# Kernel tuning notes

Measured on AMD Instinct MI355X. Metric: run time of the kernel, lower is better.

## Reference

```python
import jax, jax.numpy as jnp
import numpy as np

CTX = 768   # ctx_len in the original module
C = 768     # n_embd
B = 16
T = 768
K_EPS = 1e-8


def setup_inputs() -> dict:
    key = jax.random.key(0)
    ks = jax.random.split(key, 10)
    scale = 1.0 / np.sqrt(C)
    x = jax.random.normal(ks[0], (B, T, C), jnp.float32)
    time_decay = jax.random.normal(ks[1], (C, 1), jnp.float32) * 0.1
    time_first = jnp.full((C, 1), np.log(0.3), jnp.float32)
    time_mix_k = jax.random.uniform(ks[2], (1, 1, C), jnp.float32)
    time_mix_v = jax.random.uniform(ks[3], (1, 1, C), jnp.float32)
    time_mix_r = jax.random.uniform(ks[4], (1, 1, C), jnp.float32)
    Wk = jax.random.normal(ks[5], (C, C), jnp.float32) * scale
    Wv = jax.random.normal(ks[6], (C, C), jnp.float32) * scale
    Wr = jax.random.normal(ks[7], (C, C), jnp.float32) * scale
    Wo = jax.random.normal(ks[8], (C, C), jnp.float32) * scale
    return {"x": x, "time_decay": time_decay, "time_first": time_first,
            "time_mix_k": time_mix_k, "time_mix_v": time_mix_v, "time_mix_r": time_mix_r,
            "Wk": Wk, "Wv": Wv, "Wr": Wr, "Wo": Wo}


def reference(x, time_decay, time_first, time_mix_k, time_mix_v, time_mix_r, Wk, Wv, Wr, Wo):
    Bb, Tt, Cc = x.shape
    # time_shift: xx[t] = x[t-1], xx[0] = 0
    xx = jnp.pad(x, ((0, 0), (1, 0), (0, 0)))[:, :Tt]
    xk = x * time_mix_k + xx * (1.0 - time_mix_k)
    xv = x * time_mix_v + xx * (1.0 - time_mix_v)
    xr = x * time_mix_r + xx * (1.0 - time_mix_r)
    # projections (nn.Linear, no bias: y = x @ W.T); k, v laid out [B, C, T]
    k = jnp.einsum('btc,oc->bot', xk, Wk)
    v = jnp.einsum('btc,oc->bot', xv, Wv)
    r = jnp.einsum('btc,oc->bto', xr, Wr)
    k = jnp.exp(jnp.minimum(k, 60.0))
    kv = k * v
    # decay kernel: time_w = cat([exp(time_decay)*time_curve, time_first]); w = exp(time_w)[:, -T:]
    curve = (jnp.arange(CTX - 1) - (CTX - 2)).astype(x.dtype)  # [-(CTX-2) .. 0]
    tw = jnp.concatenate([jnp.exp(time_decay) * curve[None, :], time_first], axis=-1)  # [C, CTX]
    w = jnp.exp(tw)[:, -Tt:]            # [C, T]
    kern = w[:, None, :]                # [C, 1, T] depthwise kernel

    def causal_conv(z):  # z: [B, C, T] -> [B, C, T], left-padded cross-correlation
        return jax.lax.conv_general_dilated(
            z, kern, window_strides=(1,), padding=[(Tt - 1, 0)],
            feature_group_count=Cc, dimension_numbers=('NCH', 'OIH', 'NCH'))

    wkv = causal_conv(kv)
    wk = causal_conv(k) + K_EPS
    rwkv = jax.nn.sigmoid(r) * jnp.transpose(wkv / wk, (0, 2, 1))  # [B, T, C]
    return jnp.einsum('btc,oc->bto', rwkv, Wo)
```

## Files before the change

### kernel.cpp

```cpp
#include <hip/hip_runtime.h>
#include <math.h>

#define Mq 12288
#define Nq 768
#define Kq 768
#define Tq 768
#define Bq 16
#define Cq 768
#define BK 64
#define BM 128

typedef __bf16 bf16x8 __attribute__((ext_vector_type(8)));
typedef __bf16 bf16x4 __attribute__((ext_vector_type(4)));
typedef __bf16 bf16x2 __attribute__((ext_vector_type(2)));
typedef float  floatx4 __attribute__((ext_vector_type(4)));

#define GLD_LDS16(g, l) __builtin_amdgcn_global_load_lds(                      \
    (const __attribute__((address_space(1))) unsigned int*)(g),                \
    (__attribute__((address_space(3))) unsigned int*)(l), 16, 0, 0)

__global__ __launch_bounds__(256)
void prep_kernel(const float* __restrict__ x,
                 const float* __restrict__ mk, const float* __restrict__ mv,
                 const float* __restrict__ mr,
                 const float* __restrict__ Wk, const float* __restrict__ Wv,
                 const float* __restrict__ Wr, const float* __restrict__ Wo,
                 __bf16* __restrict__ xk, __bf16* __restrict__ xv,
                 __bf16* __restrict__ xr, __bf16* __restrict__ wp)
{
    const int bid = blockIdx.x;
    if (bid < 9216) {
        const int i  = bid * 256 + threadIdx.x;
        const int c4 = i % (Cq / 4);
        const int m  = i / (Cq / 4);
        const int t  = m % Tq;
        const int c0 = c4 * 4;

        const float4 xc = *(const float4*)(x + (size_t)m * Cq + c0);
        float4 xp = make_float4(0.f, 0.f, 0.f, 0.f);
        if (t > 0) xp = *(const float4*)(x + (size_t)(m - 1) * Cq + c0);

        const float4 k4 = *(const float4*)(mk + c0);
        const float4 v4 = *(const float4*)(mv + c0);
        const float4 r4 = *(const float4*)(mr + c0);

        bf16x4 ok = { (__bf16)fmaf(k4.x, xc.x - xp.x, xp.x),
                      (__bf16)fmaf(k4.y, xc.y - xp.y, xp.y),
                      (__bf16)fmaf(k4.z, xc.z - xp.z, xp.z),
                      (__bf16)fmaf(k4.w, xc.w - xp.w, xp.w) };
        bf16x4 ov = { (__bf16)fmaf(v4.x, xc.x - xp.x, xp.x),
                      (__bf16)fmaf(v4.y, xc.y - xp.y, xp.y),
                      (__bf16)fmaf(v4.z, xc.z - xp.z, xp.z),
                      (__bf16)fmaf(v4.w, xc.w - xp.w, xp.w) };
        bf16x4 orr = { (__bf16)fmaf(r4.x, xc.x - xp.x, xp.x),
                       (__bf16)fmaf(r4.y, xc.y - xp.y, xp.y),
                       (__bf16)fmaf(r4.z, xc.z - xp.z, xp.z),
                       (__bf16)fmaf(r4.w, xc.w - xp.w, xp.w) };
        const size_t o = (size_t)m * Cq + c0;
        *(bf16x4*)(xk + o) = ok;
        *(bf16x4*)(xv + o) = ov;
        *(bf16x4*)(xr + o) = orr;
    } else {
        const int i   = (bid - 9216) * 256 + threadIdx.x;
        const int a   = i / 147456;
        const int off = (i - a * 147456) * 4;
        const float* s = (a == 0) ? Wk : (a == 1) ? Wv : (a == 2) ? Wr : Wo;
        const float4 v = *(const float4*)(s + off);
        bf16x4 r = { (__bf16)v.x, (__bf16)v.y, (__bf16)v.z, (__bf16)v.w };
        *(bf16x4*)(wp + (size_t)a * 589824 + off) = r;
    }
}

template<bool KVR>
__global__ __launch_bounds__(256, 3)
void mfma_gemm(const __bf16* __restrict__ A0, const __bf16* __restrict__ A1,
               const __bf16* __restrict__ A2,
               const __bf16* __restrict__ W,
               __bf16* __restrict__ OUTb, float* __restrict__ OUTf)
{
    __shared__ __bf16 As[BM * BK];
    __shared__ __bf16 Bs[128 * BK];

    const int STRIPS = KVR ? 18 : 6;

    const int i_    = blockIdx.x;
    const int xcd   = i_ & 7;
    const int j_    = i_ >> 3;
    const int strip = j_ % STRIPS;
    const int mt    = xcd * 12 + j_ / STRIPS;

    const int tid   = threadIdx.x;
    const int wave  = tid >> 6;
    const int lane  = tid & 63;
    const int m0    = mt * BM;
    const int matid = KVR ? strip / 6 : 0;
    const int n0    = KVR ? (strip % 6) * 128 : strip * 128;
    const int wn0   = strip * 128;

    const __bf16* A = KVR ? (matid == 0 ? A0 : matid == 1 ? A1 : A2) : A0;

    const int r8 = lane >> 3;
    const int sc = (lane & 7) ^ r8;
    const __bf16* gA[4];  __bf16* lA[4];
    const __bf16* gB[4];  __bf16* lB[4];
#pragma unroll
    for (int i = 0; i < 4; ++i) {
        const int row = (wave * 4 + i) * 8 + r8;
        gA[i] = A + (size_t)(m0 + row) * Kq + sc * 8;
        lA[i] = As + (wave * 4 + i) * 512;
        gB[i] = W + (size_t)(wn0 + row) * Kq + sc * 8;
        lB[i] = Bs + (wave * 4 + i) * 512;
    }

    const int wm   = wave & 1;
    const int wn   = wave >> 1;
    const int xRow = wm * 64 + (lane & 15);
    const int wRow = wn * 64 + (lane & 15);
    const int lk   = lane >> 4;

    floatx4 acc[4][4];
#pragma unroll
    for (int i = 0; i < 4; ++i)
#pragma unroll
        for (int j = 0; j < 4; ++j) acc[i][j] = (floatx4){0.f, 0.f, 0.f, 0.f};

    for (int kt = 0; kt < Kq / BK; ++kt) {
#pragma unroll
        for (int i = 0; i < 4; ++i) { GLD_LDS16(gA[i], lA[i]); gA[i] += BK; }
#pragma unroll
        for (int i = 0; i < 4; ++i) { GLD_LDS16(gB[i], lB[i]); gB[i] += BK; }
        __syncthreads();

#pragma unroll
        for (int kk = 0; kk < 2; ++kk) {
            bf16x8 wF[4], xF[4];
#pragma unroll
            for (int i = 0; i < 4; ++i) {
                const int r = wRow + i * 16;
                wF[i] = *(const bf16x8*)(Bs + r * BK +
                                         (((kk << 2) | lk) ^ (r & 7)) * 8);
            }
#pragma unroll
            for (int j = 0; j < 4; ++j) {
                const int r = xRow + j * 16;
                xF[j] = *(const bf16x8*)(As + r * BK +
                                         (((kk << 2) | lk) ^ (r & 7)) * 8);
            }
#pragma unroll
            for (int i = 0; i < 4; ++i)
#pragma unroll
                for (int j = 0; j < 4; ++j)
                    acc[i][j] = __builtin_amdgcn_mfma_f32_16x16x32_bf16(
                        wF[i], xF[j], acc[i][j], 0, 0, 0);
        }
        __syncthreads();
    }

#pragma unroll
    for (int j = 0; j < 4; ++j) {
        const int tok = m0 + wm * 64 + j * 16 + (lane & 15);
#pragma unroll
        for (int i = 0; i < 4; ++i) {
            const int ch = n0 + wn * 64 + i * 16 + (lane >> 4) * 4;
            if (KVR) {
                float v0 = acc[i][j][0], v1 = acc[i][j][1];
                float v2 = acc[i][j][2], v3 = acc[i][j][3];
                if (matid == 0) {
                    v0 = expf(fminf(v0, 60.f)); v1 = expf(fminf(v1, 60.f));
                    v2 = expf(fminf(v2, 60.f)); v3 = expf(fminf(v3, 60.f));
                } else if (matid == 2) {
                    v0 = 1.f / (1.f + expf(-v0)); v1 = 1.f / (1.f + expf(-v1));
                    v2 = 1.f / (1.f + expf(-v2)); v3 = 1.f / (1.f + expf(-v3));
                }
                bf16x4 o = { (__bf16)v0, (__bf16)v1, (__bf16)v2, (__bf16)v3 };
                *(bf16x4*)(OUTb + (size_t)matid * Mq * Nq +
                           (size_t)tok * Nq + ch) = o;
            } else {
                floatx4 o = acc[i][j];
                *(floatx4*)(OUTf + (size_t)tok * Nq + ch) = o;
            }
        }
    }
}

#define SEG 16
#define SLEN (Tq / SEG)

__global__ __launch_bounds__(1024)
void scan_kernel(const __bf16* __restrict__ kb, const __bf16* __restrict__ vb,
                 __bf16* rb,
                 const float* __restrict__ td, const float* __restrict__ tf)
{
    __shared__ float2 aS[SEG][64];
    __shared__ float2 bS[SEG][64];

    const int cx  = threadIdx.x;
    const int seg = threadIdx.y;
    const int c0  = blockIdx.x * 128 + cx * 2;
    const int b   = blockIdx.y;

    const float d0 = expf(td[c0]),     d1 = expf(td[c0 + 1]);
    const float w0 = expf(-d0),        w1 = expf(-d1);
    const float u0 = expf(tf[c0]),     u1 = expf(tf[c0 + 1]);

    const size_t base = ((size_t)b * Tq + seg * SLEN) * Cq + c0;

    float a0 = 0.f, a1 = 0.f, s0 = 0.f, s1 = 0.f;
#pragma unroll 4
    for (int t = 0; t < SLEN; ++t) {
        const size_t idx = base + (size_t)t * Cq;
        const bf16x2 k2 = *(const bf16x2*)(kb + idx);
        const bf16x2 v2 = *(const bf16x2*)(vb + idx);
        const float k0 = (float)k2[0], k1 = (float)k2[1];
        a0 = fmaf(w0, a0, k0 * (float)v2[0]);
        a1 = fmaf(w1, a1, k1 * (float)v2[1]);
        s0 = fmaf(w0, s0, k0);
        s1 = fmaf(w1, s1, k1);
    }
    aS[seg][cx] = make_float2(a0, a1);
    bS[seg][cx] = make_float2(s0, s1);
    __syncthreads();

    if (seg == 0) {
        const float W0 = expf(-d0 * (float)SLEN);
        const float W1 = expf(-d1 * (float)SLEN);
        float ia0 = 0.f, ia1 = 0.f, ib0 = 0.f, ib1 = 0.f;
#pragma unroll
        for (int s = 0; s < SEG; ++s) {
            const float2 ta = aS[s][cx];
            const float2 tb = bS[s][cx];
            aS[s][cx] = make_float2(ia0, ia1);
            bS[s][cx] = make_float2(ib0, ib1);
            ia0 = fmaf(W0, ia0, ta.x);  ia1 = fmaf(W1, ia1, ta.y);
            ib0 = fmaf(W0, ib0, tb.x);  ib1 = fmaf(W1, ib1, tb.y);
        }
    }
    __syncthreads();

    const float2 ain = aS[seg][cx];
    const float2 bin = bS[seg][cx];
    a0 = ain.x; a1 = ain.y; s0 = bin.x; s1 = bin.y;
#pragma unroll 2
    for (int t = 0; t < SLEN; ++t) {
        const size_t idx = base + (size_t)t * Cq;
        const bf16x2 k2 = *(const bf16x2*)(kb + idx);
        const bf16x2 v2 = *(const bf16x2*)(vb + idx);
        const bf16x2 r2 = *(const bf16x2*)(rb + idx);
        const float k0 = (float)k2[0], k1 = (float)k2[1];
        const float kv0 = k0 * (float)v2[0], kv1 = k1 * (float)v2[1];
        const float n0 = fmaf(u0, kv0, a0), n1 = fmaf(u1, kv1, a1);
        const float e0 = fmaf(u0, k0, s0) + 1e-8f;
        const float e1 = fmaf(u1, k1, s1) + 1e-8f;
        bf16x2 o = { (__bf16)((float)r2[0] * n0 / e0),
                     (__bf16)((float)r2[1] * n1 / e1) };
        *(bf16x2*)(rb + idx) = o;
        a0 = fmaf(w0, a0, kv0);  a1 = fmaf(w1, a1, kv1);
        s0 = fmaf(w0, s0, k0);   s1 = fmaf(w1, s1, k1);
    }
}

extern "C" void kernel_launch(void* const* d_in, const int* in_sizes, int n_in,
                              void* d_out, int out_size, void* d_ws, size_t ws_size,
                              hipStream_t stream)
{
    const float* x  = (const float*)d_in[0];
    const float* td = (const float*)d_in[1];
    const float* tf = (const float*)d_in[2];
    const float* mk = (const float*)d_in[3];
    const float* mv = (const float*)d_in[4];
    const float* mr = (const float*)d_in[5];
    const float* Wk = (const float*)d_in[6];
    const float* Wv = (const float*)d_in[7];
    const float* Wr = (const float*)d_in[8];
    const float* Wo = (const float*)d_in[9];

    const size_t MC = (size_t)Mq * Cq;

    __bf16* xk = (__bf16*)d_out;
    __bf16* xv = xk + MC;

    __bf16* xr   = (__bf16*)d_ws;
    __bf16* kbuf = xr + MC;
    __bf16* vbuf = kbuf + MC;
    __bf16* rbuf = vbuf + MC;
    __bf16* Wp   = rbuf + MC;
    __bf16* Wob  = Wp + 3 * 589824;

    prep_kernel<<<11520, 256, 0, stream>>>(x, mk, mv, mr, Wk, Wv, Wr, Wo,
                                           xk, xv, xr, Wp);

    mfma_gemm<true><<<18 * 96, 256, 0, stream>>>(
        xk, xv, xr, Wp, kbuf, nullptr);

    scan_kernel<<<dim3(Cq / 128, Bq), dim3(64, SEG), 0, stream>>>(
        kbuf, vbuf, rbuf, td, tf);

    mfma_gemm<false><<<6 * 96, 256, 0, stream>>>(
        rbuf, nullptr, nullptr, Wob, nullptr, (float*)d_out);
}
```

Measured before the change: 227.2 us.

## Triple-buffer GEMM LDS with 8-wave 128x256 tiles and split-phase prefetch

The bf16 MFMA GEMM goes from 256-thread 128x128 tiles with a single LDS buffer and full syncs to 512-thread 128x256 tiles. A three-stage ring of LDS buffers is filled by direct global-to-LDS loads issued two K-steps ahead, split across two half-steps with explicit vmcnt waits and barriers. s_setprio brackets the MFMA bursts. This hides global-load latency and halves the number of blocks, at the cost of more LDS per block, lower occupancy and tighter synchronisation that may be fragile.

New measurement: 243.4 us. 7.1% more time.

```diff
diff --git a/kernel.cpp b/kernel.cpp
--- a/kernel.cpp
+++ b/kernel.cpp
@@ -9,6 +9,9 @@
 #define Cq 768
 #define BK 64
 #define BM 128
+#define BN 256
+#define KT (Kq / BK)
+#define BUFE 24576
 
 typedef __bf16 bf16x8 __attribute__((ext_vector_type(8)));
 typedef __bf16 bf16x4 __attribute__((ext_vector_type(4)));
@@ -72,16 +75,15 @@
 }
 
 template<bool KVR>
-__global__ __launch_bounds__(256, 3)
+__global__ __launch_bounds__(512, 2)
 void mfma_gemm(const __bf16* __restrict__ A0, const __bf16* __restrict__ A1,
                const __bf16* __restrict__ A2,
                const __bf16* __restrict__ W,
                __bf16* __restrict__ OUTb, float* __restrict__ OUTf)
 {
-    __shared__ __bf16 As[BM * BK];
-    __shared__ __bf16 Bs[128 * BK];
-
-    const int STRIPS = KVR ? 18 : 6;
+    __shared__ __bf16 LDS[3 * BUFE];
+
+    const int STRIPS = KVR ? 9 : 3;
 
     const int i_    = blockIdx.x;
     const int xcd   = i_ & 7;
@@ -90,33 +92,37 @@
     const int mt    = xcd * 12 + j_ / STRIPS;
 
     const int tid   = threadIdx.x;
-    const int wave  = tid >> 6;
+    const int wv    = tid >> 6;
     const int lane  = tid & 63;
     const int m0    = mt * BM;
-    const int matid = KVR ? strip / 6 : 0;
-    const int n0    = KVR ? (strip % 6) * 128 : strip * 128;
-    const int wn0   = strip * 128;
-
-    const __bf16* A = KVR ? (matid == 0 ? A0 : matid == 1 ? A1 : A2) : A0;
+    const int matid = KVR ? strip / 3 : 0;
+    const int n0    = (KVR ? strip % 3 : strip) * BN;
+
+    const __bf16* X  = KVR ? (matid == 0 ? A0 : matid == 1 ? A1 : A2) : A0;
+    const __bf16* Wb = W + (size_t)(matid * 768 + n0) * Kq;
 
     const int r8 = lane >> 3;
     const int sc = (lane & 7) ^ r8;
-    const __bf16* gA[4];  __bf16* lA[4];
-    const __bf16* gB[4];  __bf16* lB[4];
+    const __bf16* gW[4];  int lW[4];
+    const __bf16* gX[2];  int lX[2];
 #pragma unroll
     for (int i = 0; i < 4; ++i) {
-        const int row = (wave * 4 + i) * 8 + r8;
-        gA[i] = A + (size_t)(m0 + row) * Kq + sc * 8;
-        lA[i] = As + (wave * 4 + i) * 512;
-        gB[i] = W + (size_t)(wn0 + row) * Kq + sc * 8;
-        lB[i] = Bs + (wave * 4 + i) * 512;
-    }
-
-    const int wm   = wave & 1;
-    const int wn   = wave >> 1;
-    const int xRow = wm * 64 + (lane & 15);
-    const int wRow = wn * 64 + (lane & 15);
-    const int lk   = lane >> 4;
+        const int row = (wv * 4 + i) * 8 + r8;
+        gW[i] = Wb + (size_t)row * Kq + sc * 8;
+        lW[i] = (wv * 4 + i) * 512;
+    }
+#pragma unroll
+    for (int i = 0; i < 2; ++i) {
+        const int row = (wv * 2 + i) * 8 + r8;
+        gX[i] = X + (size_t)(m0 + row) * Kq + sc * 8;
+        lX[i] = 16384 + (wv * 2 + i) * 512;
+    }
+
+    const int wn  = wv & 3;
+    const int wm  = wv >> 2;
+    const int rW0 = wn * 64 + (lane & 15);
+    const int rX0 = wm * 64 + (lane & 15);
+    const int lk  = lane >> 4;
 
     floatx4 acc[4][4];
 #pragma unroll
@@ -124,36 +130,73 @@
 #pragma unroll
         for (int j = 0; j < 4; ++j) acc[i][j] = (floatx4){0.f, 0.f, 0.f, 0.f};
 
-    for (int kt = 0; kt < Kq / BK; ++kt) {
-#pragma unroll
-        for (int i = 0; i < 4; ++i) { GLD_LDS16(gA[i], lA[i]); gA[i] += BK; }
-#pragma unroll
-        for (int i = 0; i < 4; ++i) { GLD_LDS16(gB[i], lB[i]); gB[i] += BK; }
-        __syncthreads();
-
-#pragma unroll
-        for (int kk = 0; kk < 2; ++kk) {
-            bf16x8 wF[4], xF[4];
-#pragma unroll
-            for (int i = 0; i < 4; ++i) {
-                const int r = wRow + i * 16;
-                wF[i] = *(const bf16x8*)(Bs + r * BK +
-                                         (((kk << 2) | lk) ^ (r & 7)) * 8);
-            }
-#pragma unroll
-            for (int j = 0; j < 4; ++j) {
-                const int r = xRow + j * 16;
-                xF[j] = *(const bf16x8*)(As + r * BK +
-                                         (((kk << 2) | lk) ^ (r & 7)) * 8);
-            }
-#pragma unroll
-            for (int i = 0; i < 4; ++i)
-#pragma unroll
-                for (int j = 0; j < 4; ++j)
-                    acc[i][j] = __builtin_amdgcn_mfma_f32_16x16x32_bf16(
-                        wF[i], xF[j], acc[i][j], 0, 0, 0);
-        }
-        __syncthreads();
+#pragma unroll
+    for (int b = 0; b < 2; ++b) {
+        __bf16* Lb = LDS + b * BUFE;
+#pragma unroll
+        for (int i = 0; i < 4; ++i) GLD_LDS16(gW[i] + b * BK, Lb + lW[i]);
+#pragma unroll
+        for (int i = 0; i < 2; ++i) GLD_LDS16(gX[i] + b * BK, Lb + lX[i]);
+    }
+    asm volatile("s_waitcnt vmcnt(6)" ::: "memory");
+    __builtin_amdgcn_s_barrier();
+
+    for (int kt = 0; kt < KT; ++kt) {
+        const __bf16* LW = LDS + (kt % 3) * BUFE;
+        const __bf16* LX = LW + 16384;
+        const int bs = (kt + 2) % 3;
+        const int ks = (kt + 2) % KT;
+        __bf16* Lb = LDS + bs * BUFE;
+
+        bf16x8 wF[4], xF[4];
+#pragma unroll
+        for (int i = 0; i < 4; ++i) {
+            const int r = rW0 + i * 16;
+            wF[i] = *(const bf16x8*)(LW + r * BK + (lk ^ (r & 7)) * 8);
+        }
+#pragma unroll
+        for (int j = 0; j < 4; ++j) {
+            const int r = rX0 + j * 16;
+            xF[j] = *(const bf16x8*)(LX + r * BK + (lk ^ (r & 7)) * 8);
+        }
+        GLD_LDS16(gW[0] + ks * BK, Lb + lW[0]);
+        GLD_LDS16(gW[1] + ks * BK, Lb + lW[1]);
+        GLD_LDS16(gX[0] + ks * BK, Lb + lX[0]);
+        __builtin_amdgcn_s_barrier();
+        __builtin_amdgcn_s_setprio(1);
+#pragma unroll
+        for (int i = 0; i < 4; ++i)
+#pragma unroll
+            for (int j = 0; j < 4; ++j)
+                acc[i][j] = __builtin_amdgcn_mfma_f32_16x16x32_bf16(
+                    wF[i], xF[j], acc[i][j], 0, 0, 0);
+        __builtin_amdgcn_s_setprio(0);
+        __builtin_amdgcn_s_barrier();
+
+#pragma unroll
+        for (int i = 0; i < 4; ++i) {
+            const int r = rW0 + i * 16;
+            wF[i] = *(const bf16x8*)(LW + r * BK + ((4 | lk) ^ (r & 7)) * 8);
+        }
+#pragma unroll
+        for (int j = 0; j < 4; ++j) {
+            const int r = rX0 + j * 16;
+            xF[j] = *(const bf16x8*)(LX + r * BK + ((4 | lk) ^ (r & 7)) * 8);
+        }
+        GLD_LDS16(gW[2] + ks * BK, Lb + lW[2]);
+        GLD_LDS16(gW[3] + ks * BK, Lb + lW[3]);
+        GLD_LDS16(gX[1] + ks * BK, Lb + lX[1]);
+        asm volatile("s_waitcnt vmcnt(6)" ::: "memory");
+        __builtin_amdgcn_s_barrier();
+        __builtin_amdgcn_s_setprio(1);
+#pragma unroll
+        for (int i = 0; i < 4; ++i)
+#pragma unroll
+            for (int j = 0; j < 4; ++j)
+                acc[i][j] = __builtin_amdgcn_mfma_f32_16x16x32_bf16(
+                    wF[i], xF[j], acc[i][j], 0, 0, 0);
+        __builtin_amdgcn_s_setprio(0);
+        __builtin_amdgcn_s_barrier();
     }
 
 #pragma unroll
@@ -289,12 +332,12 @@
     prep_kernel<<<11520, 256, 0, stream>>>(x, mk, mv, mr, Wk, Wv, Wr, Wo,
                                            xk, xv, xr, Wp);
 
-    mfma_gemm<true><<<18 * 96, 256, 0, stream>>>(
+    mfma_gemm<true><<<9 * 96, 512, 0, stream>>>(
         xk, xv, xr, Wp, kbuf, nullptr);
 
     scan_kernel<<<dim3(Cq / 128, Bq), dim3(64, SEG), 0, stream>>>(
         kbuf, vbuf, rbuf, td, tf);
 
-    mfma_gemm<false><<<6 * 96, 256, 0, stream>>>(
+    mfma_gemm<false><<<3 * 96, 512, 0, stream>>>(
         rbuf, nullptr, nullptr, Wob, nullptr, (float*)d_out);
 }
```
